# Optimization experiments

Hardware: AMD Instinct MI355X
Metric: run time of the kernel (lower is better)

## Reference

```python
import jax, jax.numpy as jnp
import numpy as np

BS = 2048   # batch, iterated sequentially (memory carried step to step)
M = 256     # memory_size
E = 128     # expanded_memory_emb_size
HS = 512    # summarizer_hidden_size
HA = 512    # shared_AC_hidden_size
HP = 256    # processor_hidden_size


def make_pe(max_len, d):
    # standard sinusoidal positional encoding [max_len, d]
    pos = np.arange(max_len, dtype=np.float32)[:, None]
    div = np.exp(np.arange(0, d, 2, dtype=np.float32) * (-np.log(10000.0) / d))
    pe = np.zeros((max_len, d), dtype=np.float32)
    pe[:, 0::2] = np.sin(pos * div)
    pe[:, 1::2] = np.cos(pos * div)
    return jnp.asarray(pe)


def setup_inputs() -> dict:
    key = jax.random.key(0)
    ks = jax.random.split(key, 32)

    def n(k, sh, s=0.05):
        return jax.random.normal(k, sh, dtype=jnp.float32) * s

    return {
        "state": jax.random.normal(ks[0], (BS, 4), dtype=jnp.float32),
        "memory0": jax.random.uniform(ks[1], (M, E), dtype=jnp.float32),  # buffer init U(0,1)
        # embedder: Linear(4, E)
        "W_emb": n(ks[2], (4, E)), "b_emb": n(ks[3], (E,)),
        # reader Summarizer MLP: E -> HS -> 1
        "Wr1": n(ks[4], (E, HS)), "br1": n(ks[5], (HS,)),
        "Wr2": n(ks[6], (HS, 1)), "br2": n(ks[7], (1,)),
        # writer Summarizer MLP: E -> HS -> M
        "Ww1": n(ks[8], (E, HS)), "bw1": n(ks[9], (HS,)),
        "Ww2": n(ks[10], (HS, M)), "bw2": n(ks[11], (M,)),
        # shared AC trunk: 2E -> HA
        "Ws": n(ks[12], (2 * E, HA)), "bs_": n(ks[13], (HA,)),
        # actor: HA -> 5, critic: HA -> 1
        "Wa": n(ks[14], (HA, 5)), "ba": n(ks[15], (5,)),
        "Wc": n(ks[16], (HA, 1)), "bc": n(ks[17], (1,)),
        # processor: (5 + 1 + 2E) -> HP -> E
        "Wp1": n(ks[18], (5 + 1 + 2 * E, HP)), "bp1": n(ks[19], (HP,)),
        "Wp2": n(ks[20], (HP, E)), "bp2": n(ks[21], (E,)),
    }


def reference(state, memory0, W_emb, b_emb, Wr1, br1, Wr2, br2,
              Ww1, bw1, Ww2, bw2, Ws, bs_, Wa, ba, Wc, bc,
              Wp1, bp1, Wp2, bp2):
    pe_mem = make_pe(M, E)  # PE added to the M memory slots
    sg = jax.lax.stop_gradient

    def summarize(x, W1, b1, W2, b2):
        # Summarizer (MLP method): weight = softmax over token axis, z = weight^T x
        w = jax.nn.softmax(jax.nn.relu(x @ W1 + b1) @ W2 + b2, axis=0)  # [T, K]
        return w.T @ x  # [K, E]

    se = state @ W_emb + b_emb  # embed once: [BS, E]

    def step(mem, s):
        # reader over [current state ; PE(memory)] -> single summary token
        xr = jnp.concatenate([s[None, :], mem + pe_mem], axis=0)        # [M+1, E]
        mem_state = summarize(xr, Wr1, br1, Wr2, br2)[0]                # [E]
        cstate = jnp.concatenate([s, mem_state])                        # concat=True -> [2E]
        h = jax.nn.relu(cstate @ Ws + bs_)                              # [HA]
        probs = jax.nn.softmax(h @ Wa + ba)                             # [5]
        val = h @ Wc + bc                                               # [1]
        pin = jnp.concatenate([s, mem_state, probs, val])               # [2E+6]
        ms2 = jax.nn.relu(pin @ Wp1 + bp1) @ Wp2 + bp2                  # processed mem_state [E]
        # writer sees detached state / mem_state / memory (torch .detach())
        xw = jnp.concatenate([sg(s)[None, :], sg(ms2)[None, :], sg(mem) + pe_mem], axis=0)  # [M+2, E]
        nm = summarize(xw, Ww1, bw1, Ww2, bw2)                          # [M, E]
        nm = nm - nm.min(axis=-1, keepdims=True)
        nm = nm / nm.max(axis=-1, keepdims=True)
        return nm, (probs, val)

    _, (action_probs, state_values) = jax.lax.scan(step, memory0, se)
    return action_probs, state_values  # [BS, 5], [BS, 1]
```

## Files before the change

kernel.cpp:

```cpp
#include <hip/hip_runtime.h>
#include <math.h>

#define BSZ 2048
#define MM  256
#define EE  128
#define HSS 512
#define HPP 256
#define NOWN 64
#define NBLK 129
#define LEADER 128
#define TPB 512
#define ROWS 4

typedef float f4 __attribute__((ext_vector_type(4)));

#define MSQ_IDX   0
#define ROWQ(g)   ((1+(g))*32)
#define SCQ(g)    ((65+(g))*32)
#define OFF_ES    4160
#define OFF_BD    8256
#define OFF_PE    10304
#define OFF_R0    (OFF_PE + MM*EE)
#define OFF_W0    (OFF_R0 + BSZ)
#define OFF_MP    (OFF_W0 + BSZ*MM)
#define OFF_SW    (OFF_MP + 2*MM*EE)
#define OFF_EV    (OFF_SW + 2*MM*MM)
#define OFF_CS    (OFF_EV + NOWN*EE)
#define OFF_CBS   (OFF_CS + 4*HSS)
#define OFF_CP    (OFF_CBS + HSS)
#define OFF_CBP   (OFF_CP + 4*HPP)
#define OFF_MS2   (OFF_CBP + HPP)
#define OFF_BP    (OFF_MS2 + EE)

struct KParams {
  const float *state, *mem0, *Wemb, *bemb, *Wr1, *br1, *Wr2, *br2;
  const float *Ww1, *bw1, *Ww2, *bw2, *Ws, *bs, *Wa, *ba, *Wc, *bc;
  const float *Wp1, *bp1, *Wp2, *bp2;
  float *out;
  float *ws;
};

__device__ __forceinline__ float ldA(const float* p) {
  return __hip_atomic_load(p, __ATOMIC_RELAXED, __HIP_MEMORY_SCOPE_AGENT);
}
__device__ __forceinline__ void stA(float* p, float v) {
  __hip_atomic_store(p, v, __ATOMIC_RELAXED, __HIP_MEMORY_SCOPE_AGENT);
}
__device__ __forceinline__ unsigned ldAu(const unsigned* p) {
  return __hip_atomic_load(p, __ATOMIC_RELAXED, __HIP_MEMORY_SCOPE_AGENT);
}
__device__ __forceinline__ void stAu(unsigned* p, unsigned v) {
  __hip_atomic_store(p, v, __ATOMIC_RELAXED, __HIP_MEMORY_SCOPE_AGENT);
}

__device__ __forceinline__ void ldA4x8(const float* p, int strideF, f4* v) {
  const float *p1=p+strideF, *p2=p+2*strideF, *p3=p+3*strideF,
              *p4=p+4*strideF, *p5=p+5*strideF, *p6=p+6*strideF, *p7=p+7*strideF;
  asm volatile(
    "global_load_dwordx4 %0, %8, off sc0 sc1\n\t"
    "global_load_dwordx4 %1, %9, off sc0 sc1\n\t"
    "global_load_dwordx4 %2, %10, off sc0 sc1\n\t"
    "global_load_dwordx4 %3, %11, off sc0 sc1\n\t"
    "global_load_dwordx4 %4, %12, off sc0 sc1\n\t"
    "global_load_dwordx4 %5, %13, off sc0 sc1\n\t"
    "global_load_dwordx4 %6, %14, off sc0 sc1\n\t"
    "global_load_dwordx4 %7, %15, off sc0 sc1\n\t"
    "s_waitcnt vmcnt(0)"
    : "=&v"(v[0]), "=&v"(v[1]), "=&v"(v[2]), "=&v"(v[3]),
      "=&v"(v[4]), "=&v"(v[5]), "=&v"(v[6]), "=&v"(v[7])
    : "v"(p), "v"(p1), "v"(p2), "v"(p3), "v"(p4), "v"(p5), "v"(p6), "v"(p7)
    : "memory");
}
__device__ __forceinline__ void ldA4x4(const float* p, int strideF, f4* v) {
  const float *p1=p+strideF, *p2=p+2*strideF, *p3=p+3*strideF;
  asm volatile(
    "global_load_dwordx4 %0, %4, off sc0 sc1\n\t"
    "global_load_dwordx4 %1, %5, off sc0 sc1\n\t"
    "global_load_dwordx4 %2, %6, off sc0 sc1\n\t"
    "global_load_dwordx4 %3, %7, off sc0 sc1\n\t"
    "s_waitcnt vmcnt(0)"
    : "=&v"(v[0]), "=&v"(v[1]), "=&v"(v[2]), "=&v"(v[3])
    : "v"(p), "v"(p1), "v"(p2), "v"(p3)
    : "memory");
}
__device__ __forceinline__ f4 ldA4(const float* p) {
  f4 r;
  asm volatile("global_load_dwordx4 %0, %1, off sc0 sc1\n\ts_waitcnt vmcnt(0)"
    : "=&v"(r) : "v"(p) : "memory");
  return r;
}

__device__ __forceinline__ void drainSync() {
  asm volatile("s_waitcnt vmcnt(0)" ::: "memory");
  __syncthreads();
}

__device__ __forceinline__ float brs(float v, float* s8, int tid) {
  for (int o = 32; o > 0; o >>= 1) v += __shfl_down(v, o, 64);
  __syncthreads();
  if ((tid & 63) == 0) s8[tid >> 6] = v;
  __syncthreads();
  float r = s8[0]+s8[1]+s8[2]+s8[3]+s8[4]+s8[5]+s8[6]+s8[7];
  __syncthreads();
  return r;
}

template<int N>
__device__ __forceinline__ void brsN(float* v, float* sred, int tid) {
  #pragma unroll
  for (int k = 0; k < N; ++k)
    for (int o = 32; o > 0; o >>= 1) v[k] += __shfl_down(v[k], o, 64);
  __syncthreads();
  if ((tid & 63) == 0) {
    const int w = tid >> 6;
    #pragma unroll
    for (int k = 0; k < N; ++k) sred[k*8 + w] = v[k];
  }
  __syncthreads();
  #pragma unroll
  for (int k = 0; k < N; ++k) {
    float s = sred[k*8 + 0];
    #pragma unroll
    for (int w = 1; w < 8; ++w) s += sred[k*8 + w];
    v[k] = s;
  }
  __syncthreads();
}

__global__ __launch_bounds__(TPB)
void toyac_kernel(KParams p) {
  const int g = blockIdx.x;
  const int tid = threadIdx.x;
  float* ws = p.ws;
  unsigned* bar = (unsigned*)p.ws;
  const int isOwner = (g < NOWN);
  const int og = (g >= NOWN && g < LEADER) ? (g - NOWN) : g;
  const int c0 = ROWS * ((g < NOWN) ? g : og);

  __shared__ float sBuf[8192];
  __shared__ float sH4[ROWS][HSS];
  __shared__ float sX[ROWS][EE];
  __shared__ float sP[ROWS][EE];
  __shared__ float sPE[ROWS][EE];
  __shared__ float sHv[HSS];
  __shared__ float sMS[EE];
  __shared__ float sMS2[EE];
  __shared__ float sSE[EE];
  __shared__ float sP1[HPP];
  __shared__ float sD[ROWS];
  __shared__ float sR48[48];
  __shared__ float s8[8];
  __shared__ float sRed[16];
  __shared__ float sSm[40];

  float (*sEv)[MM] = (float(*)[MM])sH4;

  const int hq = (tid & 127) * 4;
  const int eg4 = tid >> 7;

  if (isOwner) {
    const int e = tid & 127, r = tid >> 7, c = c0 + r;
    double dv = exp(-(double)(2*(e>>1)) * log(10000.0) / 128.0);
    double arg = (double)c * dv;
    float pev = ((e & 1) == 0) ? (float)sin(arg) : (float)cos(arg);
    sPE[r][e] = pev;
    float m0v = p.mem0[(size_t)c*EE + e] + pev;
    stA(ws + OFF_MP + (size_t)c*EE + e, m0v);
    sX[r][e] = m0v;
  } else if (g == LEADER) {
    for (int jj = tid; jj < HSS; jj += TPB) {
      float a0=0.f,a1=0.f,a2=0.f,a3=0.f,cb=0.f;
      for (int e = 0; e < EE; ++e) {
        float wv = p.Ws[(size_t)e*HSS + jj];
        a0 += p.Wemb[e]*wv; a1 += p.Wemb[EE+e]*wv;
        a2 += p.Wemb[2*EE+e]*wv; a3 += p.Wemb[3*EE+e]*wv;
        cb += p.bemb[e]*wv;
      }
      ws[OFF_CS + jj] = a0; ws[OFF_CS + HSS + jj] = a1;
      ws[OFF_CS + 2*HSS + jj] = a2; ws[OFF_CS + 3*HSS + jj] = a3;
      ws[OFF_CBS + jj] = cb;
    }
    if (tid < HPP) {
      int k = tid;
      float a0=0.f,a1=0.f,a2=0.f,a3=0.f,cb=0.f;
      for (int e = 0; e < EE; ++e) {
        float wv = p.Wp1[(size_t)e*HPP + k];
        a0 += p.Wemb[e]*wv; a1 += p.Wemb[EE+e]*wv;
        a2 += p.Wemb[2*EE+e]*wv; a3 += p.Wemb[3*EE+e]*wv;
        cb += p.bemb[e]*wv;
      }
      ws[OFF_CP + k] = a0; ws[OFF_CP + HPP + k] = a1;
      ws[OFF_CP + 2*HPP + k] = a2; ws[OFF_CP + 3*HPP + k] = a3;
      ws[OFF_CBP + k] = cb;
    }
  }

  for (int t = g; t < BSZ; t += NBLK) {
    __syncthreads();
    if (tid < EE) {
      const float* st = p.state + (size_t)t*4;
      sSE[tid] = st[0]*p.Wemb[tid] + st[1]*p.Wemb[EE+tid]
               + st[2]*p.Wemb[2*EE+tid] + st[3]*p.Wemb[3*EE+tid] + p.bemb[tid];
    }
    __syncthreads();
    {
      f4 a = {0.f,0.f,0.f,0.f};
      const float* base = p.Wr1 + (size_t)(eg4*32)*HSS + hq;
      for (int i = 0; i < 32; ++i)
        a += sSE[eg4*32 + i] * (*(const f4*)(base + (size_t)i*HSS));
      *(f4*)(sBuf + (size_t)eg4*HSS + hq) = a;
      __syncthreads();
      int h = tid;
      float hid = sBuf[h] + sBuf[HSS+h] + sBuf[2*HSS+h] + sBuf[3*HSS+h] + p.br1[h];
      float v = fmaxf(hid, 0.f) * p.Wr2[h];
      float sc = brs(v, s8, tid);
      if (tid == 0) stA(ws + OFF_R0 + t, sc + p.br2[0]);
      __syncthreads();
    }
    {
      f4 a = {0.f,0.f,0.f,0.f};
      const float* base = p.Ww1 + (size_t)(eg4*32)*HSS + hq;
      for (int i = 0; i < 32; ++i)
        a += sSE[eg4*32 + i] * (*(const f4*)(base + (size_t)i*HSS));
      *(f4*)(sBuf + (size_t)eg4*HSS + hq) = a;
      __syncthreads();
      int h = tid;
      sHv[h] = fmaxf(sBuf[h] + sBuf[HSS+h] + sBuf[2*HSS+h] + sBuf[3*HSS+h] + p.bw1[h], 0.f);
      __syncthreads();
      const int cq = (tid & 63) * 4, hg = tid >> 6;
      f4 q = {0.f,0.f,0.f,0.f};
      const float* b2 = p.Ww2 + (size_t)(hg*64)*MM + cq;
      for (int i = 0; i < 64; ++i)
        q += sHv[hg*64 + i] * (*(const f4*)(b2 + (size_t)i*MM));
      *(f4*)(sBuf + (size_t)hg*MM + cq) = q;
      __syncthreads();
      if (tid < MM) {
        float s = 0.f;
        #pragma unroll
        for (int k = 0; k < 8; ++k) s += sBuf[(size_t)k*MM + tid];
        stA(ws + OFF_W0 + (size_t)t*MM + tid, s + p.bw2[tid]);
      }
      __syncthreads();
    }
  }

  auto stageA = [&](float* esSumOut) {
    {
      f4 a0={0.f,0.f,0.f,0.f},a1=a0,a2=a0,a3=a0;
      const float* base = p.Wr1 + (size_t)(eg4*32)*HSS + hq;
      for (int i = 0; i < 32; ++i) {
        f4 w = *(const f4*)(base + (size_t)i*HSS);
        int e = eg4*32 + i;
        a0 += sX[0][e]*w; a1 += sX[1][e]*w; a2 += sX[2][e]*w; a3 += sX[3][e]*w;
      }
      *(f4*)(sBuf + ((size_t)eg4*ROWS + 0)*HSS + hq) = a0;
      *(f4*)(sBuf + ((size_t)eg4*ROWS + 1)*HSS + hq) = a1;
      *(f4*)(sBuf + ((size_t)eg4*ROWS + 2)*HSS + hq) = a2;
      *(f4*)(sBuf + ((size_t)eg4*ROWS + 3)*HSS + hq) = a3;
    }
    __syncthreads();
    float sc[ROWS];
    {
      int h = tid;
      float b = p.br1[h], wr = p.Wr2[h];
      #pragma unroll
      for (int r = 0; r < ROWS; ++r) {
        float hid = sBuf[(0*ROWS+r)*HSS+h] + sBuf[(1*ROWS+r)*HSS+h]
                  + sBuf[(2*ROWS+r)*HSS+h] + sBuf[(3*ROWS+r)*HSS+h] + b;
        sc[r] = fmaxf(hid, 0.f) * wr;
      }
      brsN<ROWS>(sc, sR48, tid);
    }
    float es[ROWS];
    #pragma unroll
    for (int r = 0; r < ROWS; ++r) es[r] = expf(sc[r] + p.br2[0]);
    if (tid < EE) {
      float v = es[0]*sX[0][tid] + es[1]*sX[1][tid] + es[2]*sX[2][tid] + es[3]*sX[3][tid];
      stA(ws + OFF_EV + (size_t)g*EE + tid, v);
    }
    *esSumOut = es[0]+es[1]+es[2]+es[3];
  };

  auto ww2pass = [&](float* swdst) {
    const int cq = (tid & 63) * 4, hg = tid >> 6;
    f4 q0={0.f,0.f,0.f,0.f},q1=q0,q2=q0,q3=q0;
    const float* b2 = p.Ww2 + (size_t)(hg*64)*MM + cq;
    for (int i = 0; i < 64; ++i) {
      f4 w = *(const f4*)(b2 + (size_t)i*MM);
      int h = hg*64 + i;
      q0 += sH4[0][h]*w; q1 += sH4[1][h]*w; q2 += sH4[2][h]*w; q3 += sH4[3][h]*w;
    }
    *(f4*)(sBuf + ((size_t)hg*ROWS + 0)*MM + cq) = q0;
    *(f4*)(sBuf + ((size_t)hg*ROWS + 1)*MM + cq) = q1;
    *(f4*)(sBuf + ((size_t)hg*ROWS + 2)*MM + cq) = q2;
    *(f4*)(sBuf + ((size_t)hg*ROWS + 3)*MM + cq) = q3;
    __syncthreads();
    {
      const int col = tid & 255, rp = tid >> 8;
      #pragma unroll
      for (int rr = 0; rr < 2; ++rr) {
        int r = rp*2 + rr;
        float s = 0.f;
        #pragma unroll
        for (int k = 0; k < 8; ++k) s += sBuf[((size_t)k*ROWS + r)*MM + col];
        stA(swdst + (size_t)(c0 + r)*MM + col, s + p.bw2[col]);
      }
    }
  };

  auto stageC = [&](float* swdst) {
    {
      f4 a0={0.f,0.f,0.f,0.f},a1=a0,a2=a0,a3=a0;
      const float* base = p.Ww1 + (size_t)(eg4*32)*HSS + hq;
      for (int i = 0; i < 32; ++i) {
        f4 w = *(const f4*)(base + (size_t)i*HSS);
        int e = eg4*32 + i;
        a0 += sX[0][e]*w; a1 += sX[1][e]*w; a2 += sX[2][e]*w; a3 += sX[3][e]*w;
      }
      *(f4*)(sBuf + ((size_t)eg4*ROWS + 0)*HSS + hq) = a0;
      *(f4*)(sBuf + ((size_t)eg4*ROWS + 1)*HSS + hq) = a1;
      *(f4*)(sBuf + ((size_t)eg4*ROWS + 2)*HSS + hq) = a2;
      *(f4*)(sBuf + ((size_t)eg4*ROWS + 3)*HSS + hq) = a3;
    }
    __syncthreads();
    {
      int h = tid;
      float b = p.bw1[h];
      #pragma unroll
      for (int r = 0; r < ROWS; ++r)
        sH4[r][h] = fmaxf(sBuf[(0*ROWS+r)*HSS+h] + sBuf[(1*ROWS+r)*HSS+h]
                        + sBuf[(2*ROWS+r)*HSS+h] + sBuf[(3*ROWS+r)*HSS+h] + b, 0.f);
    }
    __syncthreads();
    ww2pass(swdst);
  };

  auto dBulkH = [&](int tt) {
    float* swc = ws + OFF_SW + (size_t)(tt&1)*MM*MM;
    float* mpc = ws + OFF_MP + (size_t)(tt&1)*MM*EE;
    float ex[ROWS] = {0.f,0.f,0.f,0.f};
    if (tid < MM) {
      f4 s = ldA4(swc + (size_t)tid*MM + c0);
      #pragma unroll
      for (int r = 0; r < ROWS; ++r) { ex[r] = expf(s[r]); sEv[r][tid] = ex[r]; }
    }
    brsN<ROWS>(ex, sR48, tid);
    if (tid == 0) { sD[0]=ex[0]; sD[1]=ex[1]; sD[2]=ex[2]; sD[3]=ex[3]; }
    {
      const int e4 = (tid & 31) * 4, rg = tid >> 5;
      f4 a0={0.f,0.f,0.f,0.f},a1=a0,a2=a0,a3=a0;
      const float* base = mpc + (size_t)(rg*16)*EE + e4;
      f4 vv[8];
      ldA4x8(base, EE, vv);
      #pragma unroll
      for (int i = 0; i < 8; ++i) {
        int r0 = rg*16 + i;
        a0 += sEv[0][r0]*vv[i]; a1 += sEv[1][r0]*vv[i];
        a2 += sEv[2][r0]*vv[i]; a3 += sEv[3][r0]*vv[i];
      }
      ldA4x8(base + 8*EE, EE, vv);
      #pragma unroll
      for (int i = 0; i < 8; ++i) {
        int r0 = rg*16 + 8 + i;
        a0 += sEv[0][r0]*vv[i]; a1 += sEv[1][r0]*vv[i];
        a2 += sEv[2][r0]*vv[i]; a3 += sEv[3][r0]*vv[i];
      }
      *(f4*)(sBuf + ((size_t)0*16 + rg)*EE + e4) = a0;
      *(f4*)(sBuf + ((size_t)1*16 + rg)*EE + e4) = a1;
      *(f4*)(sBuf + ((size_t)2*16 + rg)*EE + e4) = a2;
      *(f4*)(sBuf + ((size_t)3*16 + rg)*EE + e4) = a3;
    }
    __syncthreads();
    {
      const int e = tid & 127, r = tid >> 7;
      float s = 0.f;
      #pragma unroll
      for (int q = 0; q < 16; ++q) s += sBuf[((size_t)r*16 + q)*EE + e];
      stA(ws + OFF_BP + ((size_t)og*ROWS + r)*EE + e, s);
    }
  };

  if (g == LEADER) {
    for (int t = 0; t < BSZ; ++t) {
      float er0 = expf(ldA(ws + OFF_R0 + t));
      float v = 0.f;
      if (tid < NOWN) {
        float* es = ws + OFF_ES + (size_t)((t&1)*NOWN + tid)*32;
        do { v = ldA(es); } while (v == 0.f);
        stA(es, 0.f);
      }
      float invd = 1.f / (er0 + brs(v, s8, tid));
      {
        const int e4 = (tid & 31) * 4, qg = tid >> 5;
        f4 vv[4];
        ldA4x4(ws + OFF_EV + (size_t)(qg*4)*EE + e4, EE, vv);
        f4 acc = vv[0]+vv[1]+vv[2]+vv[3];
        *(f4*)(sBuf + (size_t)qg*EE + e4) = acc;
      }
      __syncthreads();
      {
        const float* st = p.state + (size_t)t*4;
        const float s0 = st[0], s1 = st[1], s2 = st[2], s3 = st[3];
        if (tid < EE) {
          float se = s0*p.Wemb[tid] + s1*p.Wemb[EE+tid]
                   + s2*p.Wemb[2*EE+tid] + s3*p.Wemb[3*EE+tid] + p.bemb[tid];
          float s = 0.f;
          #pragma unroll
          for (int q = 0; q < 16; ++q) s += sBuf[(size_t)q*EE + tid];
          sMS[tid] = (er0*se + s) * invd;
        }
        __syncthreads();
        {
          f4 a = {0.f,0.f,0.f,0.f};
          const float* base = p.Ws + (size_t)(EE + eg4*32)*HSS + hq;
          for (int i = 0; i < 32; ++i)
            a += sMS[eg4*32 + i] * (*(const f4*)(base + (size_t)i*HSS));
          *(f4*)(sBuf + (size_t)eg4*HSS + hq) = a;
        }
        __syncthreads();
        float hv;
        {
          const float* cs = ws + OFF_CS;
          float sh0 = s0*cs[tid] + s1*cs[HSS+tid] + s2*cs[2*HSS+tid] + s3*cs[3*HSS+tid]
                    + ws[OFF_CBS + tid];
          hv = fmaxf(sBuf[tid] + sBuf[HSS+tid] + sBuf[2*HSS+tid] + sBuf[3*HSS+tid]
                     + sh0 + p.bs[tid], 0.f);
        }
        __syncthreads();
        {
          float pa[6];
          #pragma unroll
          for (int aa = 0; aa < 5; ++aa) pa[aa] = hv * p.Wa[(size_t)tid*5 + aa];
          pa[5] = hv * p.Wc[tid];
          brsN<6>(pa, sR48, tid);
          if (tid == 0) {
            float l0=pa[0]+p.ba[0], l1=pa[1]+p.ba[1], l2=pa[2]+p.ba[2];
            float l3=pa[3]+p.ba[3], l4=pa[4]+p.ba[4];
            float mx = fmaxf(fmaxf(fmaxf(l0,l1),fmaxf(l2,l3)), l4);
            float e0=expf(l0-mx),e1=expf(l1-mx),e2=expf(l2-mx),e3=expf(l3-mx),e4v=expf(l4-mx);
            float is = 1.f/(e0+e1+e2+e3+e4v);
            float p0=e0*is,p1=e1*is,p2=e2*is,p3=e3*is,p4=e4v*is;
            p.out[(size_t)t*5+0]=p0; p.out[(size_t)t*5+1]=p1; p.out[(size_t)t*5+2]=p2;
            p.out[(size_t)t*5+3]=p3; p.out[(size_t)t*5+4]=p4;
            float val = pa[5] + p.bc[0];
            p.out[(size_t)BSZ*5 + t] = val;
            sSm[1]=p0; sSm[2]=p1; sSm[3]=p2; sSm[4]=p3; sSm[5]=p4; sSm[6]=val;
          }
          __syncthreads();
        }
        {
          const int cq = (tid & 63) * 4, eg8 = tid >> 6;
          f4 a = {0.f,0.f,0.f,0.f};
          const float* base = p.Wp1 + (size_t)(EE + eg8*16)*HPP + cq;
          for (int i = 0; i < 16; ++i)
            a += sMS[eg8*16 + i] * (*(const f4*)(base + (size_t)i*HPP));
          *(f4*)(sBuf + (size_t)eg8*HPP + cq) = a;
        }
        __syncthreads();
        if (tid < HPP) {
          const float* cp = ws + OFF_CP;
          float acc = s0*cp[tid] + s1*cp[HPP+tid] + s2*cp[2*HPP+tid] + s3*cp[3*HPP+tid]
                    + ws[OFF_CBP + tid] + p.bp1[tid];
          #pragma unroll
          for (int q = 0; q < 8; ++q) acc += sBuf[(size_t)q*HPP + tid];
          #pragma unroll
          for (int aa = 0; aa < 5; ++aa) acc += sSm[1+aa] * p.Wp1[(size_t)(2*EE+aa)*HPP + tid];
          acc += sSm[6] * p.Wp1[(size_t)(2*EE+5)*HPP + tid];
          sP1[tid] = fmaxf(acc, 0.f);
        }
        __syncthreads();
        {
          const int cq = (tid & 31) * 4, kg = tid >> 5;
          f4 a = {0.f,0.f,0.f,0.f};
          const float* base = p.Wp2 + (size_t)(kg*16)*EE + cq;
          for (int i = 0; i < 16; ++i)
            a += sP1[kg*16 + i] * (*(const f4*)(base + (size_t)i*EE));
          *(f4*)(sBuf + (size_t)kg*EE + cq) = a;
        }
        __syncthreads();
        if (tid < EE) {
          float s = 0.f;
          #pragma unroll
          for (int q = 0; q < 16; ++q) s += sBuf[(size_t)q*EE + tid];
          stA(ws + OFF_MS2 + tid, s + p.bp2[tid]);
        }
      }
      drainSync();
      if (tid == 0) stAu(&bar[MSQ_IDX], (unsigned)(t+1));
    }
  } else if (isOwner) {
    const f4 wcol = *(const f4*)(p.Ww2 + (size_t)tid*MM + c0);
    const float rBw1v = p.bw1[tid];
    drainSync();
    if (tid == 0) stAu(&bar[ROWQ(g)], 1u);
    float esSum;
    stageA(&esSum);
    drainSync();
    if (tid == 0) stA(ws + OFF_ES + (size_t)g*32, esSum);

    for (int t = 0; t < BSZ-1; ++t) {
      if (tid < EE) {
        const float* st = p.state + (size_t)t*4;
        sSE[tid] = st[0]*p.Wemb[tid] + st[1]*p.Wemb[EE+tid]
                 + st[2]*p.Wemb[2*EE+tid] + st[3]*p.Wemb[3*EE+tid] + p.bemb[tid];
      }
      if (tid == 0) {
        f4 w0 = ldA4(ws + OFF_W0 + (size_t)t*MM + c0);
        sSm[8]=expf(w0.x); sSm[9]=expf(w0.y); sSm[10]=expf(w0.z); sSm[11]=expf(w0.w);
      }
      if (tid == 0) { while (ldAu(&bar[MSQ_IDX]) < (unsigned)(t+1)) {} }
      __syncthreads();
      if (tid < EE) sMS2[tid] = ldA(ws + OFF_MS2 + tid);
      if (tid == 0) {
        float* bd = ws + OFF_BD + (size_t)g*32;
        float x,y,z,w;
        do { x=ldA(bd); y=ldA(bd+1); z=ldA(bd+2); w=ldA(bd+3); }
        while (x==0.f || y==0.f || z==0.f || w==0.f);
        sD[0]=x; sD[1]=y; sD[2]=z; sD[3]=w;
        stA(bd,0.f); stA(bd+1,0.f); stA(bd+2,0.f); stA(bd+3,0.f);
      }
      __syncthreads();
      {
        const int e = tid & 127, r = tid >> 7;
        sP[r][e] = ldA(ws + OFF_BP + ((size_t)g*ROWS + r)*EE + e);
      }
      {
        f4 a = {0.f,0.f,0.f,0.f};
        const float* base = p.Ww1 + (size_t)(eg4*32)*HSS + hq;
        for (int i = 0; i < 32; ++i)
          a += sMS2[eg4*32 + i] * (*(const f4*)(base + (size_t)i*HSS));
        *(f4*)(sBuf + (size_t)eg4*HSS + hq) = a;
      }
      __syncthreads();
      float hm = fmaxf(sBuf[tid] + sBuf[HSS+tid] + sBuf[2*HSS+tid] + sBuf[3*HSS+tid]
                       + rBw1v, 0.f);
      __syncthreads();
      float swv[ROWS] = { hm*wcol.x, hm*wcol.y, hm*wcol.z, hm*wcol.w };
      brsN<ROWS>(swv, sR48, tid);
      {
        const int e = tid & 127, r = tid >> 7;
        float ew1 = expf(swv[r] + p.bw2[c0+r]);
        float ew0 = sSm[8+r];
        float inv = 1.f / (sD[r] + ew0 + ew1);
        float x = (sP[r][e] + ew0*sSE[e] + ew1*sMS2[e]) * inv;
        float mn = x, mx = x;
        #pragma unroll
        for (int o = 1; o < 64; o <<= 1) {
          mn = fminf(mn, __shfl_xor(mn, o, 64));
          mx = fmaxf(mx, __shfl_xor(mx, o, 64));
        }
        if ((tid & 63) == 0) { sRed[(tid>>6)*2] = mn; sRed[(tid>>6)*2+1] = mx; }
        __syncthreads();
        mn = fminf(sRed[4*r], sRed[4*r+2]);
        mx = fmaxf(sRed[4*r+1], sRed[4*r+3]);
        float k = 1.f / (mx - mn);
        float xr = (x - mn) * k + sPE[r][e];
        stA(ws + OFF_MP + (size_t)((t+1)&1)*MM*EE + (size_t)(c0+r)*EE + e, xr);
        sX[r][e] = xr;
      }
      drainSync();
      if (tid == 0) stAu(&bar[ROWQ(g)], (unsigned)(t+2));
      stageA(&esSum);
      drainSync();
      if (tid == 0) stA(ws + OFF_ES + (size_t)(((t+1)&1)*NOWN + g)*32, esSum);
    }
  } else {
    for (int t = 0; t < BSZ-1; ++t) {
      if (tid == 0) {
        while (ldAu(&bar[ROWQ(og)]) < (unsigned)(t+1)) __builtin_amdgcn_s_sleep(2);
      }
      __syncthreads();
      {
        const int e = tid & 127, r = tid >> 7;
        sX[r][e] = ldA(ws + OFF_MP + (size_t)(t&1)*MM*EE + (size_t)(c0+r)*EE + e);
      }
      __syncthreads();
      stageC(ws + OFF_SW + (size_t)(t&1)*MM*MM);
      drainSync();
      if (tid == 0) stAu(&bar[SCQ(og)], (unsigned)(t+1));
      if (tid < 64) {
        while (ldAu(&bar[SCQ(tid)]) < (unsigned)(t+1)) __builtin_amdgcn_s_sleep(2);
      } else if (tid < 128) {
        while (ldAu(&bar[ROWQ(tid-64)]) < (unsigned)(t+1)) __builtin_amdgcn_s_sleep(2);
      }
      __syncthreads();
      dBulkH(t);
      drainSync();
      if (tid == 0) {
        float* bd = ws + OFF_BD + (size_t)og*32;
        stA(bd,   sD[0]); stA(bd+1, sD[1]);
        stA(bd+2, sD[2]); stA(bd+3, sD[3]);
      }
    }
  }
}

extern "C" void kernel_launch(void* const* d_in, const int* in_sizes, int n_in,
                              void* d_out, int out_size, void* d_ws, size_t ws_size,
                              hipStream_t stream) {
  hipMemsetAsync(d_ws, 0, OFF_PE * 4, stream);
  KParams kp;
  kp.state = (const float*)d_in[0];
  kp.mem0  = (const float*)d_in[1];
  kp.Wemb  = (const float*)d_in[2];
  kp.bemb  = (const float*)d_in[3];
  kp.Wr1   = (const float*)d_in[4];
  kp.br1   = (const float*)d_in[5];
  kp.Wr2   = (const float*)d_in[6];
  kp.br2   = (const float*)d_in[7];
  kp.Ww1   = (const float*)d_in[8];
  kp.bw1   = (const float*)d_in[9];
  kp.Ww2   = (const float*)d_in[10];
  kp.bw2   = (const float*)d_in[11];
  kp.Ws    = (const float*)d_in[12];
  kp.bs    = (const float*)d_in[13];
  kp.Wa    = (const float*)d_in[14];
  kp.ba    = (const float*)d_in[15];
  kp.Wc    = (const float*)d_in[16];
  kp.bc    = (const float*)d_in[17];
  kp.Wp1   = (const float*)d_in[18];
  kp.bp1   = (const float*)d_in[19];
  kp.Wp2   = (const float*)d_in[20];
  kp.bp2   = (const float*)d_in[21];
  kp.out   = (float*)d_out;
  kp.ws    = (float*)d_ws;
  toyac_kernel<<<dim3(NBLK), dim3(TPB), 0, stream>>>(kp);
}
```

Measured before the change: 50.27 ms.

## Keep leader and owner weight slices resident in registers across timesteps

The leader block now preloads its column of the Ws memory-half and a 64-row slice of Wp2 into per-thread registers once, then computes the trunk and processor dot products straight from registers. This removes the per-step global weight reads and one split-K reduction plus its barriers. Owner blocks likewise keep a 128-entry column of Wr1 in registers and compute the reader hidden layer without the shared-memory partial-sum pass and its barrier. The cost is very high register pressure (about 190 floats per thread on the leader), which may spill or lower occupancy on this persistent, latency-bound sequential kernel.

```diff
diff --git a/kernel.cpp b/kernel.cpp
--- a/kernel.cpp
+++ b/kernel.cpp
@@ -244,43 +244,6 @@
     }
   }
 
-  auto stageA = [&](float* esSumOut) {
-    {
-      f4 a0={0.f,0.f,0.f,0.f},a1=a0,a2=a0,a3=a0;
-      const float* base = p.Wr1 + (size_t)(eg4*32)*HSS + hq;
-      for (int i = 0; i < 32; ++i) {
-        f4 w = *(const f4*)(base + (size_t)i*HSS);
-        int e = eg4*32 + i;
-        a0 += sX[0][e]*w; a1 += sX[1][e]*w; a2 += sX[2][e]*w; a3 += sX[3][e]*w;
-      }
-      *(f4*)(sBuf + ((size_t)eg4*ROWS + 0)*HSS + hq) = a0;
-      *(f4*)(sBuf + ((size_t)eg4*ROWS + 1)*HSS + hq) = a1;
-      *(f4*)(sBuf + ((size_t)eg4*ROWS + 2)*HSS + hq) = a2;
-      *(f4*)(sBuf + ((size_t)eg4*ROWS + 3)*HSS + hq) = a3;
-    }
-    __syncthreads();
-    float sc[ROWS];
-    {
-      int h = tid;
-      float b = p.br1[h], wr = p.Wr2[h];
-      #pragma unroll
-      for (int r = 0; r < ROWS; ++r) {
-        float hid = sBuf[(0*ROWS+r)*HSS+h] + sBuf[(1*ROWS+r)*HSS+h]
-                  + sBuf[(2*ROWS+r)*HSS+h] + sBuf[(3*ROWS+r)*HSS+h] + b;
-        sc[r] = fmaxf(hid, 0.f) * wr;
-      }
-      brsN<ROWS>(sc, sR48, tid);
-    }
-    float es[ROWS];
-    #pragma unroll
-    for (int r = 0; r < ROWS; ++r) es[r] = expf(sc[r] + p.br2[0]);
-    if (tid < EE) {
-      float v = es[0]*sX[0][tid] + es[1]*sX[1][tid] + es[2]*sX[2][tid] + es[3]*sX[3][tid];
-      stA(ws + OFF_EV + (size_t)g*EE + tid, v);
-    }
-    *esSumOut = es[0]+es[1]+es[2]+es[3];
-  };
-
   auto ww2pass = [&](float* swdst) {
     const int cq = (tid & 63) * 4, hg = tid >> 6;
     f4 q0={0.f,0.f,0.f,0.f},q1=q0,q2=q0,q3=q0;
@@ -381,6 +344,14 @@
   };
 
   if (g == LEADER) {
+    float wsReg[EE];
+    #pragma unroll
+    for (int e = 0; e < EE; ++e) wsReg[e] = p.Ws[(size_t)(EE + e)*HSS + tid];
+    float wp2Reg[64];
+    const int ecol = tid & 127, kq = tid >> 7;
+    #pragma unroll
+    for (int i = 0; i < 64; ++i) wp2Reg[i] = p.Wp2[(size_t)(kq*64 + i)*EE + ecol];
+
     for (int t = 0; t < BSZ; ++t) {
       float er0 = expf(ldA(ws + OFF_R0 + t));
       float v = 0.f;
@@ -410,23 +381,16 @@
           sMS[tid] = (er0*se + s) * invd;
         }
         __syncthreads();
-        {
-          f4 a = {0.f,0.f,0.f,0.f};
-          const float* base = p.Ws + (size_t)(EE + eg4*32)*HSS + hq;
-          for (int i = 0; i < 32; ++i)
-            a += sMS[eg4*32 + i] * (*(const f4*)(base + (size_t)i*HSS));
-          *(f4*)(sBuf + (size_t)eg4*HSS + hq) = a;
-        }
-        __syncthreads();
         float hv;
         {
+          float acc = 0.f;
+          #pragma unroll
+          for (int e = 0; e < EE; ++e) acc += sMS[e] * wsReg[e];
           const float* cs = ws + OFF_CS;
           float sh0 = s0*cs[tid] + s1*cs[HSS+tid] + s2*cs[2*HSS+tid] + s3*cs[3*HSS+tid]
                     + ws[OFF_CBS + tid];
-          hv = fmaxf(sBuf[tid] + sBuf[HSS+tid] + sBuf[2*HSS+tid] + sBuf[3*HSS+tid]
-                     + sh0 + p.bs[tid], 0.f);
-        }
-        __syncthreads();
+          hv = fmaxf(acc + sh0 + p.bs[tid], 0.f);
+        }
         {
           float pa[6];
           #pragma unroll
@@ -470,18 +434,14 @@
         }
         __syncthreads();
         {
-          const int cq = (tid & 31) * 4, kg = tid >> 5;
-          f4 a = {0.f,0.f,0.f,0.f};
-          const float* base = p.Wp2 + (size_t)(kg*16)*EE + cq;
-          for (int i = 0; i < 16; ++i)
-            a += sP1[kg*16 + i] * (*(const f4*)(base + (size_t)i*EE));
-          *(f4*)(sBuf + (size_t)kg*EE + cq) = a;
+          float a2 = 0.f;
+          #pragma unroll
+          for (int i = 0; i < 64; ++i) a2 += sP1[kq*64 + i] * wp2Reg[i];
+          sBuf[(size_t)kq*EE + ecol] = a2;
         }
         __syncthreads();
         if (tid < EE) {
-          float s = 0.f;
-          #pragma unroll
-          for (int q = 0; q < 16; ++q) s += sBuf[(size_t)q*EE + tid];
+          float s = sBuf[tid] + sBuf[EE+tid] + sBuf[2*EE+tid] + sBuf[3*EE+tid];
           stA(ws + OFF_MS2 + tid, s + p.bp2[tid]);
         }
       }
@@ -491,10 +451,35 @@
   } else if (isOwner) {
     const f4 wcol = *(const f4*)(p.Ww2 + (size_t)tid*MM + c0);
     const float rBw1v = p.bw1[tid];
+    float wrReg[EE];
+    #pragma unroll
+    for (int e = 0; e < EE; ++e) wrReg[e] = p.Wr1[(size_t)e*HSS + tid];
+
+    auto stageAreg = [&](float* esSumOut) {
+      float h0=0.f,h1=0.f,h2=0.f,h3=0.f;
+      #pragma unroll
+      for (int e = 0; e < EE; ++e) {
+        float w = wrReg[e];
+        h0 += sX[0][e]*w; h1 += sX[1][e]*w; h2 += sX[2][e]*w; h3 += sX[3][e]*w;
+      }
+      float b = p.br1[tid], wr = p.Wr2[tid];
+      float sc[ROWS] = { fmaxf(h0+b,0.f)*wr, fmaxf(h1+b,0.f)*wr,
+                         fmaxf(h2+b,0.f)*wr, fmaxf(h3+b,0.f)*wr };
+      brsN<ROWS>(sc, sR48, tid);
+      float es[ROWS];
+      #pragma unroll
+      for (int r = 0; r < ROWS; ++r) es[r] = expf(sc[r] + p.br2[0]);
+      if (tid < EE) {
+        float v = es[0]*sX[0][tid] + es[1]*sX[1][tid] + es[2]*sX[2][tid] + es[3]*sX[3][tid];
+        stA(ws + OFF_EV + (size_t)g*EE + tid, v);
+      }
+      *esSumOut = es[0]+es[1]+es[2]+es[3];
+    };
+
     drainSync();
     if (tid == 0) stAu(&bar[ROWQ(g)], 1u);
     float esSum;
-    stageA(&esSum);
+    stageAreg(&esSum);
     drainSync();
     if (tid == 0) stA(ws + OFF_ES + (size_t)g*32, esSum);
 
@@ -560,7 +545,7 @@
       }
       drainSync();
       if (tid == 0) stAu(&bar[ROWQ(g)], (unsigned)(t+2));
-      stageA(&esSum);
+      stageAreg(&esSum);
       drainSync();
       if (tid == 0) stA(ws + OFF_ES + (size_t)(((t+1)&1)*NOWN + g)*32, esSum);
     }
```

New measurement: 53.75 ms. +6.9%, slower.
